# Kernel optimization log

Hardware: AMD Instinct MI355X
Metric: run time of the kernel (lower is better)

## Reference

```python
import jax, jax.numpy as jnp
import numpy as np

N_ACTIVE = 200000   # active voxels
GRID = 96           # spatial grid extent per axis
C = 128             # inplanes == outplanes
EPS = 1e-4          # scn BatchNormalization default eps


def _build_rulebook(n, g, seed=0):
    """Submanifold 3x3x3 rulebook: for each of 27 offsets, pairs (in_site, out_site)
    where coord[in] = coord[out] + offset and both sites are active. Padded to
    length n with dummy index n."""
    rng = np.random.default_rng(seed)
    lin = rng.choice(g ** 3, size=n, replace=False)
    coords = np.stack(np.unravel_index(lin, (g, g, g)), axis=1)  # [n,3]
    lut = -np.ones(g ** 3, dtype=np.int64)
    lut[lin] = np.arange(n)
    in_rows, out_rows = [], []
    for dx in (-1, 0, 1):
        for dy in (-1, 0, 1):
            for dz in (-1, 0, 1):
                nb = coords + np.array([dx, dy, dz])
                valid = np.all((nb >= 0) & (nb < g), axis=1)
                j = np.full(n, -1, dtype=np.int64)
                j[valid] = lut[np.ravel_multi_index(nb[valid].T, (g, g, g))]
                hit = j >= 0
                ii = j[hit]
                oi = np.nonzero(hit)[0].astype(np.int64)
                pad = n - ii.shape[0]
                in_rows.append(np.concatenate([ii, np.full(pad, n, dtype=np.int64)]))
                out_rows.append(np.concatenate([oi, np.full(pad, n, dtype=np.int64)]))
    return np.stack(in_rows), np.stack(out_rows)  # each [27, n]


def setup_inputs() -> dict:
    key = jax.random.key(0)
    k_feat, k_w1, k_w2 = jax.random.split(key, 3)
    in_idx_np, out_idx_np = _build_rulebook(N_ACTIVE, GRID)
    w_std = 1.0 / np.sqrt(27 * C)
    return {
        "features": jax.random.normal(k_feat, (N_ACTIVE, C), dtype=jnp.float32),
        "W1": jax.random.normal(k_w1, (27, C, C), dtype=jnp.float32) * w_std,
        "gamma1": jnp.ones((C,), jnp.float32),
        "beta1": jnp.zeros((C,), jnp.float32),
        "W2": jax.random.normal(k_w2, (27, C, C), dtype=jnp.float32) * w_std,
        "gamma2": jnp.ones((C,), jnp.float32),
        "beta2": jnp.zeros((C,), jnp.float32),
        "in_idx": jnp.asarray(in_idx_np),
        "out_idx": jnp.asarray(out_idx_np),
    }


def _subm_conv(feats, W, in_idx, out_idx):
    # feats: [N, Cin]; W: [27, Cin, Cout]; rulebook idx: [27, K] (dummy = N)
    n, c_in = feats.shape
    c_out = W.shape[-1]
    feats_pad = jnp.concatenate([feats, jnp.zeros((1, c_in), feats.dtype)], axis=0)

    def step(acc, t):
        ii, oi, w = t
        contrib = feats_pad[ii] @ w  # [K, Cout] gather -> GEMM
        return acc.at[oi].add(contrib), None  # scatter-add (dummy row n absorbs pad)

    acc0 = jnp.zeros((n + 1, c_out), feats.dtype)
    acc, _ = jax.lax.scan(step, acc0, (in_idx, out_idx, W))
    return acc[:n]


def _bn(x, gamma, beta):
    # batch-norm over active sites (training-mode batch stats)
    m = x.mean(axis=0)
    v = x.var(axis=0)
    return (x - m) * jax.lax.rsqrt(v + EPS) * gamma + beta


def reference(features, W1, gamma1, beta1, W2, gamma2, beta2, in_idx, out_idx):
    out = _subm_conv(features, W1, in_idx, out_idx)
    out = jax.nn.relu(_bn(out, gamma1, beta1))          # scn.BatchNormReLU
    out = _subm_conv(out, W2, in_idx, out_idx)
    out = _bn(out, gamma2, beta2)                       # scn.BatchNormalization
    return jax.nn.relu(out + features)                  # AddTable + ReLU
```

## Files before the change

### kernel.cpp

```cpp
#include <hip/hip_runtime.h>

#define NACT 200000
#define MPAD 200064
#define NBLK 1563
#define KOFF 27

typedef __bf16 bf16x8 __attribute__((ext_vector_type(8)));
typedef __bf16 bf16x4 __attribute__((ext_vector_type(4)));
typedef float f32x4 __attribute__((ext_vector_type(4)));

__device__ __forceinline__ void async_load16(const void* g, void* l) {
  __builtin_amdgcn_global_load_lds(
      (__attribute__((address_space(1))) void*)g,
      (__attribute__((address_space(3))) void*)l, 16, 0, 0);
}

__global__ void fill_g(int* __restrict__ G) {
  int i = blockIdx.x * 256 + threadIdx.x;
  if (i < KOFF * MPAD) G[i] = NACT;
}

__global__ void scatter_g(const int* __restrict__ ii, const int* __restrict__ oi,
                          int* __restrict__ G) {
  int i = blockIdx.x * 256 + threadIdx.x;
  if (i >= KOFF * NACT) return;
  int k = i / NACT;
  int o = oi[i];
  G[k * MPAD + o] = ii[i];
}

__global__ void fix_g(int* __restrict__ G) {
  int k = threadIdx.x;
  if (k < KOFF) G[k * MPAD + NACT] = NACT;
}

__global__ void cast_feats(const float* __restrict__ F, __bf16* __restrict__ X) {
  int i = blockIdx.x * 256 + threadIdx.x;
  if (i >= (NACT + 1) * 32) return;
  float4 v = (i < NACT * 32) ? ((const float4*)F)[i] : make_float4(0.f, 0.f, 0.f, 0.f);
  bf16x4 o = {(__bf16)v.x, (__bf16)v.y, (__bf16)v.z, (__bf16)v.w};
  *(bf16x4*)(X + (i << 2)) = o;
}

__global__ void prep_w(const float* __restrict__ W1, const float* __restrict__ W2,
                       __bf16* __restrict__ T1, __bf16* __restrict__ T2) {
  int i = blockIdx.x * 256 + threadIdx.x;
  if (i >= KOFF * 128 * 128) return;
  int k = i >> 14, rem = i & 16383, n = rem >> 7, c = rem & 127;
  int src = (k << 14) + (c << 7) + n;
  T1[i] = (__bf16)W1[src];
  T2[i] = (__bf16)W2[src];
}

__global__ __launch_bounds__(256, 4) void gemm_gather(
    const __bf16* __restrict__ X,
    const __bf16* __restrict__ WT,
    const int* __restrict__ G,
    __bf16* __restrict__ Y,
    float* __restrict__ Pst)
{
  __shared__ __bf16 Alds[128 * 64];
  __shared__ __bf16 Blds[128 * 64];
  const int t = threadIdx.x;
  const int lane = t & 63;
  const int w = t >> 6;
  const int wm = (w & 1) << 6;
  const int wn = (w >> 1) << 6;
  const int m_base = blockIdx.x << 7;
  const int r0 = t >> 3;
  const int scb = t & 7;
  const int l15 = lane & 15;
  const int q4 = lane >> 4;

  f32x4 acc[4][4];
#pragma unroll
  for (int i = 0; i < 4; ++i)
#pragma unroll
    for (int j = 0; j < 4; ++j) acc[i][j] = (f32x4){0.f, 0.f, 0.f, 0.f};

  for (int kk = 0; kk < KOFF; ++kk) {
    int rowA[4];
#pragma unroll
    for (int j = 0; j < 4; ++j)
      rowA[j] = G[kk * MPAD + m_base + r0 + j * 32];
    const __bf16* wb = WT + (kk << 14);
#pragma unroll
    for (int s = 0; s < 2; ++s) {
      const int c0 = s << 6;
      __syncthreads();
#pragma unroll
      for (int j = 0; j < 4; ++j) {
        const int r = r0 + j * 32;
        const int gcb = scb ^ (r & 7);
        async_load16(wb + (r << 7) + c0 + (gcb << 3), &Blds[(((r << 3) + scb) << 3)]);
        async_load16(X + (rowA[j] << 7) + c0 + (gcb << 3), &Alds[(((r << 3) + scb) << 3)]);
      }
      __syncthreads();
#pragma unroll
      for (int ks = 0; ks < 2; ++ks) {
        bf16x8 af[4], bfr[4];
        const int cb0 = (ks << 2) + q4;
#pragma unroll
        for (int mi = 0; mi < 4; ++mi) {
          const int r = wm + mi * 16 + l15;
          af[mi] = *(const bf16x8*)&Alds[(((r << 3) + (cb0 ^ (r & 7))) << 3)];
        }
#pragma unroll
        for (int ni = 0; ni < 4; ++ni) {
          const int r = wn + ni * 16 + l15;
          bfr[ni] = *(const bf16x8*)&Blds[(((r << 3) + (cb0 ^ (r & 7))) << 3)];
        }
#pragma unroll
        for (int mi = 0; mi < 4; ++mi)
#pragma unroll
          for (int ni = 0; ni < 4; ++ni)
            acc[mi][ni] = __builtin_amdgcn_mfma_f32_16x16x32_bf16(
                af[mi], bfr[ni], acc[mi][ni], 0, 0, 0);
      }
    }
  }

#pragma unroll
  for (int mi = 0; mi < 4; ++mi) {
#pragma unroll
    for (int ni = 0; ni < 4; ++ni) {
      const int col = wn + ni * 16 + l15;
#pragma unroll
      for (int rg = 0; rg < 4; ++rg) {
        const int row = m_base + wm + mi * 16 + (q4 << 2) + rg;
        Y[(row << 7) + col] = (__bf16)acc[mi][ni][rg];
      }
    }
  }

  float s[4], s2[4];
#pragma unroll
  for (int ni = 0; ni < 4; ++ni) {
    float a = 0.f, b = 0.f;
#pragma unroll
    for (int mi = 0; mi < 4; ++mi)
#pragma unroll
      for (int rg = 0; rg < 4; ++rg) {
        float v = acc[mi][ni][rg];
        a += v; b += v * v;
      }
    s[ni] = a; s2[ni] = b;
  }
#pragma unroll
  for (int ni = 0; ni < 4; ++ni) {
    s[ni]  += __shfl_xor(s[ni], 16);  s[ni]  += __shfl_xor(s[ni], 32);
    s2[ni] += __shfl_xor(s2[ni], 16); s2[ni] += __shfl_xor(s2[ni], 32);
  }
  float* sc = (float*)Alds;
  __syncthreads();
  if (q4 == 0) {
#pragma unroll
    for (int ni = 0; ni < 4; ++ni) {
      sc[(w << 6) + ni * 16 + l15]       = s[ni];
      sc[256 + (w << 6) + ni * 16 + l15] = s2[ni];
    }
  }
  __syncthreads();
  {
    const int kind = t >> 7, col = t & 127;
    const int w1 = (col >> 6) << 1;
    const float v = sc[kind * 256 + (w1 << 6) + (col & 63)] +
                    sc[kind * 256 + ((w1 + 1) << 6) + (col & 63)];
    Pst[(size_t)t * NBLK + blockIdx.x] = v;
  }
}

__global__ void stats_reduce(const float* __restrict__ P, float* __restrict__ st) {
  int b = blockIdx.x;
  const float* p = P + (size_t)b * NBLK;
  float s = 0.f;
  for (int i = threadIdx.x; i < NBLK; i += 256) s += p[i];
  for (int off = 32; off; off >>= 1) s += __shfl_down(s, off);
  __shared__ float ls[4];
  if ((threadIdx.x & 63) == 0) ls[threadIdx.x >> 6] = s;
  __syncthreads();
  if (threadIdx.x == 0) st[b] = ls[0] + ls[1] + ls[2] + ls[3];
}

__global__ void bn_coeffs(const float* __restrict__ st, const float* __restrict__ gamma,
                          const float* __restrict__ beta, float* __restrict__ co) {
  int c = threadIdx.x;
  float m = st[c] * (1.f / NACT);
  float v = st[128 + c] * (1.f / NACT) - m * m;
  float sc = gamma[c] * rsqrtf(v + 1e-4f);
  co[c] = sc;
  co[128 + c] = beta[c] - m * sc;
}

__global__ void bn_relu_cast(const __bf16* __restrict__ Y, const float* __restrict__ co,
                             __bf16* __restrict__ X2) {
  int i = blockIdx.x * 256 + threadIdx.x;
  if (i >= (NACT + 1) * 16) return;
  bf16x8 o;
  if (i < NACT * 16) {
    bf16x8 v = ((const bf16x8*)Y)[i];
    int cg = (i & 15) << 3;
#pragma unroll
    for (int e = 0; e < 8; ++e) {
      float x = fmaf((float)v[e], co[cg + e], co[128 + cg + e]);
      o[e] = (__bf16)fmaxf(x, 0.f);
    }
  } else {
#pragma unroll
    for (int e = 0; e < 8; ++e) o[e] = (__bf16)0.f;
  }
  ((bf16x8*)X2)[i] = o;
}

__global__ void bn_add_relu(const __bf16* __restrict__ Y, const float* __restrict__ co,
                            const float* __restrict__ F, float* __restrict__ O) {
  int i = blockIdx.x * 256 + threadIdx.x;
  if (i >= NACT * 16) return;
  bf16x8 v = ((const bf16x8*)Y)[i];
  float4 f0 = ((const float4*)F)[2 * i];
  float4 f1 = ((const float4*)F)[2 * i + 1];
  int cg = (i & 15) << 3;
  float4 o0, o1;
  o0.x = fmaxf(fmaf((float)v[0], co[cg + 0], co[128 + cg + 0]) + f0.x, 0.f);
  o0.y = fmaxf(fmaf((float)v[1], co[cg + 1], co[128 + cg + 1]) + f0.y, 0.f);
  o0.z = fmaxf(fmaf((float)v[2], co[cg + 2], co[128 + cg + 2]) + f0.z, 0.f);
  o0.w = fmaxf(fmaf((float)v[3], co[cg + 3], co[128 + cg + 3]) + f0.w, 0.f);
  o1.x = fmaxf(fmaf((float)v[4], co[cg + 4], co[128 + cg + 4]) + f1.x, 0.f);
  o1.y = fmaxf(fmaf((float)v[5], co[cg + 5], co[128 + cg + 5]) + f1.y, 0.f);
  o1.z = fmaxf(fmaf((float)v[6], co[cg + 6], co[128 + cg + 6]) + f1.z, 0.f);
  o1.w = fmaxf(fmaf((float)v[7], co[cg + 7], co[128 + cg + 7]) + f1.w, 0.f);
  ((float4*)O)[2 * i] = o0;
  ((float4*)O)[2 * i + 1] = o1;
}

extern "C" void kernel_launch(void* const* d_in, const int* in_sizes, int n_in,
                              void* d_out, int out_size, void* d_ws, size_t ws_size,
                              hipStream_t stream) {
  const float* features = (const float*)d_in[0];
  const float* W1       = (const float*)d_in[1];
  const float* gamma1   = (const float*)d_in[2];
  const float* beta1    = (const float*)d_in[3];
  const float* W2       = (const float*)d_in[4];
  const float* gamma2   = (const float*)d_in[5];
  const float* beta2    = (const float*)d_in[6];
  const int* in_idx     = (const int*)d_in[7];
  const int* out_idx    = (const int*)d_in[8];

  char* ws = (char*)d_ws;
  size_t off = 0;
  int*    G   = (int*)(ws + off);    off += (size_t)KOFF * MPAD * 4;
  __bf16* X   = (__bf16*)(ws + off); off += (size_t)(NACT + 1) * 128 * 2;
  __bf16* T1  = (__bf16*)(ws + off); off += (size_t)KOFF * 128 * 128 * 2;
  __bf16* T2  = (__bf16*)(ws + off); off += (size_t)KOFF * 128 * 128 * 2;
  __bf16* Y   = (__bf16*)(ws + off); off += (size_t)MPAD * 128 * 2;
  float*  Pst = (float*)(ws + off);  off += (size_t)256 * NBLK * 4;
  float*  st  = (float*)(ws + off);  off += 4096;

  fill_g<<<(KOFF * MPAD + 255) / 256, 256, 0, stream>>>(G);
  scatter_g<<<(KOFF * NACT + 255) / 256, 256, 0, stream>>>(in_idx, out_idx, G);
  fix_g<<<1, 32, 0, stream>>>(G);
  cast_feats<<<((NACT + 1) * 32 + 255) / 256, 256, 0, stream>>>(features, X);
  prep_w<<<(KOFF * 128 * 128 + 255) / 256, 256, 0, stream>>>(W1, W2, T1, T2);

  gemm_gather<<<NBLK, 256, 0, stream>>>(X, T1, G, Y, Pst);
  stats_reduce<<<256, 256, 0, stream>>>(Pst, st);
  bn_coeffs<<<1, 128, 0, stream>>>(st, gamma1, beta1, st + 512);
  bn_relu_cast<<<((NACT + 1) * 16 + 255) / 256, 256, 0, stream>>>(Y, st + 512, X);

  gemm_gather<<<NBLK, 256, 0, stream>>>(X, T2, G, Y, Pst);
  stats_reduce<<<256, 256, 0, stream>>>(Pst, st);
  bn_coeffs<<<1, 128, 0, stream>>>(st, gamma2, beta2, st + 768);
  bn_add_relu<<<(NACT * 16 + 255) / 256, 256, 0, stream>>>(Y, st + 768, features, (float*)d_out);
}
```

Measured before the change: 616.3 us.

## Double-buffer gather GEMM stages and fuse BN stats reduction with coefficients

The gather-GEMM kernel now preloads all 27 rulebook row indices for the tile into LDS and double-buffers the A/B tiles, so async global-to-LDS loads for the next stage overlap MFMA compute on the current one. Manual vmcnt waits and sched barriers replace the per-stage syncthreads pairs. Separately, the stats reduction and BN coefficient kernels are merged into one launch. Doubling LDS per block lowers the occupancy target from 4 to 2 blocks per CU, which reduces latency hiding from extra waves.

```diff
diff --git a/kernel.cpp b/kernel.cpp
--- a/kernel.cpp
+++ b/kernel.cpp
@@ -4,6 +4,7 @@
 #define MPAD 200064
 #define NBLK 1563
 #define KOFF 27
+#define NSTAGE (KOFF * 2)
 
 typedef __bf16 bf16x8 __attribute__((ext_vector_type(8)));
 typedef __bf16 bf16x4 __attribute__((ext_vector_type(4)));
@@ -52,15 +53,19 @@
   T2[i] = (__bf16)W2[src];
 }
 
-__global__ __launch_bounds__(256, 4) void gemm_gather(
+__global__ __launch_bounds__(256, 2) void gemm_gather(
     const __bf16* __restrict__ X,
     const __bf16* __restrict__ WT,
     const int* __restrict__ G,
     __bf16* __restrict__ Y,
     float* __restrict__ Pst)
 {
-  __shared__ __bf16 Alds[128 * 64];
-  __shared__ __bf16 Blds[128 * 64];
+  __shared__ __bf16 Al0[128 * 64];
+  __shared__ __bf16 Bl0[128 * 64];
+  __shared__ __bf16 Al1[128 * 64];
+  __shared__ __bf16 Bl1[128 * 64];
+  __shared__ int Gl[KOFF * 128];
+  __shared__ float red[512];
   const int t = threadIdx.x;
   const int lane = t & 63;
   const int w = t >> 6;
@@ -78,47 +83,69 @@
 #pragma unroll
     for (int j = 0; j < 4; ++j) acc[i][j] = (f32x4){0.f, 0.f, 0.f, 0.f};
 
-  for (int kk = 0; kk < KOFF; ++kk) {
-    int rowA[4];
-#pragma unroll
-    for (int j = 0; j < 4; ++j)
-      rowA[j] = G[kk * MPAD + m_base + r0 + j * 32];
-    const __bf16* wb = WT + (kk << 14);
-#pragma unroll
-    for (int s = 0; s < 2; ++s) {
-      const int c0 = s << 6;
-      __syncthreads();
-#pragma unroll
-      for (int j = 0; j < 4; ++j) {
-        const int r = r0 + j * 32;
-        const int gcb = scb ^ (r & 7);
-        async_load16(wb + (r << 7) + c0 + (gcb << 3), &Blds[(((r << 3) + scb) << 3)]);
-        async_load16(X + (rowA[j] << 7) + c0 + (gcb << 3), &Alds[(((r << 3) + scb) << 3)]);
-      }
-      __syncthreads();
-#pragma unroll
-      for (int ks = 0; ks < 2; ++ks) {
-        bf16x8 af[4], bfr[4];
-        const int cb0 = (ks << 2) + q4;
-#pragma unroll
-        for (int mi = 0; mi < 4; ++mi) {
-          const int r = wm + mi * 16 + l15;
-          af[mi] = *(const bf16x8*)&Alds[(((r << 3) + (cb0 ^ (r & 7))) << 3)];
-        }
-#pragma unroll
-        for (int ni = 0; ni < 4; ++ni) {
-          const int r = wn + ni * 16 + l15;
-          bfr[ni] = *(const bf16x8*)&Blds[(((r << 3) + (cb0 ^ (r & 7))) << 3)];
-        }
-#pragma unroll
-        for (int mi = 0; mi < 4; ++mi)
-#pragma unroll
-          for (int ni = 0; ni < 4; ++ni)
-            acc[mi][ni] = __builtin_amdgcn_mfma_f32_16x16x32_bf16(
-                af[mi], bfr[ni], acc[mi][ni], 0, 0, 0);
-      }
-    }
-  }
+  for (int i = t; i < KOFF * 128; i += 256)
+    Gl[i] = G[(size_t)(i >> 7) * MPAD + m_base + (i & 127)];
+  __syncthreads();
+
+#define STAGE_ISSUE(sidx, AL, BL)                                              \
+  do {                                                                         \
+    const int k_ = (sidx) >> 1;                                                \
+    const int c0_ = ((sidx) & 1) << 6;                                         \
+    const __bf16* wb_ = WT + (k_ << 14);                                       \
+    _Pragma("unroll") for (int j = 0; j < 4; ++j) {                            \
+      const int r_ = r0 + j * 32;                                              \
+      const int rowA_ = Gl[(k_ << 7) + r_];                                    \
+      const int gcb_ = scb ^ (r_ & 7);                                         \
+      async_load16(wb_ + (r_ << 7) + c0_ + (gcb_ << 3),                        \
+                   &(BL)[(((r_ << 3) + scb) << 3)]);                           \
+      async_load16(X + ((size_t)rowA_ << 7) + c0_ + (gcb_ << 3),               \
+                   &(AL)[(((r_ << 3) + scb) << 3)]);                           \
+    }                                                                          \
+  } while (0)
+
+#define STAGE_COMPUTE(AL, BL)                                                  \
+  do {                                                                         \
+    _Pragma("unroll") for (int ks = 0; ks < 2; ++ks) {                         \
+      bf16x8 af[4], bfr[4];                                                    \
+      const int cb0 = (ks << 2) + q4;                                          \
+      _Pragma("unroll") for (int mi = 0; mi < 4; ++mi) {                       \
+        const int r = wm + mi * 16 + l15;                                      \
+        af[mi] = *(const bf16x8*)&(AL)[(((r << 3) + (cb0 ^ (r & 7))) << 3)];   \
+      }                                                                        \
+      _Pragma("unroll") for (int ni = 0; ni < 4; ++ni) {                       \
+        const int r = wn + ni * 16 + l15;                                      \
+        bfr[ni] = *(const bf16x8*)&(BL)[(((r << 3) + (cb0 ^ (r & 7))) << 3)];  \
+      }                                                                        \
+      _Pragma("unroll") for (int mi = 0; mi < 4; ++mi)                         \
+          _Pragma("unroll") for (int ni = 0; ni < 4; ++ni)                     \
+              acc[mi][ni] = __builtin_amdgcn_mfma_f32_16x16x32_bf16(           \
+                  af[mi], bfr[ni], acc[mi][ni], 0, 0, 0);                      \
+    }                                                                          \
+  } while (0)
+
+  STAGE_ISSUE(0, Al0, Bl0);
+  for (int s = 0; s < NSTAGE; s += 2) {
+    if (s + 1 < NSTAGE) STAGE_ISSUE(s + 1, Al1, Bl1);
+    asm volatile("s_waitcnt vmcnt(8)" ::: "memory");
+    __builtin_amdgcn_s_barrier();
+    __builtin_amdgcn_sched_barrier(0);
+    STAGE_COMPUTE(Al0, Bl0);
+    __builtin_amdgcn_sched_barrier(0);
+    __builtin_amdgcn_s_barrier();
+    if (s + 2 < NSTAGE) {
+      STAGE_ISSUE(s + 2, Al0, Bl0);
+      asm volatile("s_waitcnt vmcnt(8)" ::: "memory");
+    } else {
+      asm volatile("s_waitcnt vmcnt(0)" ::: "memory");
+    }
+    __builtin_amdgcn_s_barrier();
+    __builtin_amdgcn_sched_barrier(0);
+    STAGE_COMPUTE(Al1, Bl1);
+    __builtin_amdgcn_sched_barrier(0);
+    __builtin_amdgcn_s_barrier();
+  }
+#undef STAGE_ISSUE
+#undef STAGE_COMPUTE
 
 #pragma unroll
   for (int mi = 0; mi < 4; ++mi) {
@@ -151,45 +178,44 @@
     s[ni]  += __shfl_xor(s[ni], 16);  s[ni]  += __shfl_xor(s[ni], 32);
     s2[ni] += __shfl_xor(s2[ni], 16); s2[ni] += __shfl_xor(s2[ni], 32);
   }
-  float* sc = (float*)Alds;
   __syncthreads();
   if (q4 == 0) {
 #pragma unroll
     for (int ni = 0; ni < 4; ++ni) {
-      sc[(w << 6) + ni * 16 + l15]       = s[ni];
-      sc[256 + (w << 6) + ni * 16 + l15] = s2[ni];
+      red[(w << 6) + ni * 16 + l15]       = s[ni];
+      red[256 + (w << 6) + ni * 16 + l15] = s2[ni];
     }
   }
   __syncthreads();
   {
     const int kind = t >> 7, col = t & 127;
     const int w1 = (col >> 6) << 1;
-    const float v = sc[kind * 256 + (w1 << 6) + (col & 63)] +
-                    sc[kind * 256 + ((w1 + 1) << 6) + (col & 63)];
+    const float v = red[kind * 256 + (w1 << 6) + (col & 63)] +
+                    red[kind * 256 + ((w1 + 1) << 6) + (col & 63)];
     Pst[(size_t)t * NBLK + blockIdx.x] = v;
   }
 }
 
-__global__ void stats_reduce(const float* __restrict__ P, float* __restrict__ st) {
-  int b = blockIdx.x;
-  const float* p = P + (size_t)b * NBLK;
-  float s = 0.f;
-  for (int i = threadIdx.x; i < NBLK; i += 256) s += p[i];
-  for (int off = 32; off; off >>= 1) s += __shfl_down(s, off);
-  __shared__ float ls[4];
-  if ((threadIdx.x & 63) == 0) ls[threadIdx.x >> 6] = s;
-  __syncthreads();
-  if (threadIdx.x == 0) st[b] = ls[0] + ls[1] + ls[2] + ls[3];
-}
-
-__global__ void bn_coeffs(const float* __restrict__ st, const float* __restrict__ gamma,
-                          const float* __restrict__ beta, float* __restrict__ co) {
-  int c = threadIdx.x;
-  float m = st[c] * (1.f / NACT);
-  float v = st[128 + c] * (1.f / NACT) - m * m;
-  float sc = gamma[c] * rsqrtf(v + 1e-4f);
-  co[c] = sc;
-  co[128 + c] = beta[c] - m * sc;
+__global__ void stats_coeffs(const float* __restrict__ P, const float* __restrict__ gamma,
+                             const float* __restrict__ beta, float* __restrict__ co) {
+  int c = blockIdx.x;
+  const float* p1 = P + (size_t)c * NBLK;
+  const float* p2 = P + (size_t)(128 + c) * NBLK;
+  float s = 0.f, s2 = 0.f;
+  for (int i = threadIdx.x; i < NBLK; i += 256) { s += p1[i]; s2 += p2[i]; }
+  for (int off = 32; off; off >>= 1) { s += __shfl_down(s, off); s2 += __shfl_down(s2, off); }
+  __shared__ float ls[8];
+  if ((threadIdx.x & 63) == 0) { ls[threadIdx.x >> 6] = s; ls[4 + (threadIdx.x >> 6)] = s2; }
+  __syncthreads();
+  if (threadIdx.x == 0) {
+    float S = ls[0] + ls[1] + ls[2] + ls[3];
+    float S2 = ls[4] + ls[5] + ls[6] + ls[7];
+    float m = S * (1.f / NACT);
+    float v = S2 * (1.f / NACT) - m * m;
+    float sc = gamma[c] * rsqrtf(v + 1e-4f);
+    co[c] = sc;
+    co[128 + c] = beta[c] - m * sc;
+  }
 }
 
 __global__ void bn_relu_cast(const __bf16* __restrict__ Y, const float* __restrict__ co,
@@ -263,12 +289,10 @@
   prep_w<<<(KOFF * 128 * 128 + 255) / 256, 256, 0, stream>>>(W1, W2, T1, T2);
 
   gemm_gather<<<NBLK, 256, 0, stream>>>(X, T1, G, Y, Pst);
-  stats_reduce<<<256, 256, 0, stream>>>(Pst, st);
-  bn_coeffs<<<1, 128, 0, stream>>>(st, gamma1, beta1, st + 512);
-  bn_relu_cast<<<((NACT + 1) * 16 + 255) / 256, 256, 0, stream>>>(Y, st + 512, X);
+  stats_coeffs<<<128, 256, 0, stream>>>(Pst, gamma1, beta1, st);
+  bn_relu_cast<<<((NACT + 1) * 16 + 255) / 256, 256, 0, stream>>>(Y, st, X);
 
   gemm_gather<<<NBLK, 256, 0, stream>>>(X, T2, G, Y, Pst);
-  stats_reduce<<<256, 256, 0, stream>>>(Pst, st);
-  bn_coeffs<<<1, 128, 0, stream>>>(st, gamma2, beta2, st + 768);
-  bn_add_relu<<<(NACT * 16 + 255) / 256, 256, 0, stream>>>(Y, st + 768, features, (float*)d_out);
-}
+  stats_coeffs<<<128, 256, 0, stream>>>(Pst, gamma2, beta2, st + 256);
+  bn_add_relu<<<(NACT * 16 + 255) / 256, 256, 0, stream>>>(Y, st + 256, features, (float*)d_out);
+}
```

Result: slower. 691.4 us (+12.2%).

## Enlarge gather-GEMM M tile to 192 rows and fuse BN stats reduction kernels

Applied to the files above, without the earlier changes.

Raises the rows per block in the gather GEMM from 128 to 192, so each weight tile in LDS is reused across more gathered rows and fewer blocks are launched. Occupancy drops to 3 blocks per CU, and more accumulator registers are needed. The separate stats reduction and BN coefficient kernels are merged into one kernel per channel to cut launch overhead. A dedicated shared buffer replaces the reuse of the A tile for the reduction scratch space.

```diff
diff --git a/kernel.cpp b/kernel.cpp
--- a/kernel.cpp
+++ b/kernel.cpp
@@ -2,7 +2,8 @@
 
 #define NACT 200000
 #define MPAD 200064
-#define NBLK 1563
+#define BM 192
+#define NBLK 1042
 #define KOFF 27
 
 typedef __bf16 bf16x8 __attribute__((ext_vector_type(8)));
@@ -52,36 +53,37 @@
   T2[i] = (__bf16)W2[src];
 }
 
-__global__ __launch_bounds__(256, 4) void gemm_gather(
+__global__ __launch_bounds__(256, 3) void gemm_gather(
     const __bf16* __restrict__ X,
     const __bf16* __restrict__ WT,
     const int* __restrict__ G,
     __bf16* __restrict__ Y,
     float* __restrict__ Pst)
 {
-  __shared__ __bf16 Alds[128 * 64];
+  __shared__ __bf16 Alds[BM * 64];
   __shared__ __bf16 Blds[128 * 64];
+  __shared__ float red[512];
   const int t = threadIdx.x;
   const int lane = t & 63;
   const int w = t >> 6;
-  const int wm = (w & 1) << 6;
+  const int wm = (w & 1) * 96;
   const int wn = (w >> 1) << 6;
-  const int m_base = blockIdx.x << 7;
+  const int m_base = blockIdx.x * BM;
   const int r0 = t >> 3;
   const int scb = t & 7;
   const int l15 = lane & 15;
   const int q4 = lane >> 4;
 
-  f32x4 acc[4][4];
-#pragma unroll
-  for (int i = 0; i < 4; ++i)
+  f32x4 acc[6][4];
+#pragma unroll
+  for (int i = 0; i < 6; ++i)
 #pragma unroll
     for (int j = 0; j < 4; ++j) acc[i][j] = (f32x4){0.f, 0.f, 0.f, 0.f};
 
   for (int kk = 0; kk < KOFF; ++kk) {
-    int rowA[4];
-#pragma unroll
-    for (int j = 0; j < 4; ++j)
+    int rowA[6];
+#pragma unroll
+    for (int j = 0; j < 6; ++j)
       rowA[j] = G[kk * MPAD + m_base + r0 + j * 32];
     const __bf16* wb = WT + (kk << 14);
 #pragma unroll
@@ -93,35 +95,39 @@
         const int r = r0 + j * 32;
         const int gcb = scb ^ (r & 7);
         async_load16(wb + (r << 7) + c0 + (gcb << 3), &Blds[(((r << 3) + scb) << 3)]);
-        async_load16(X + (rowA[j] << 7) + c0 + (gcb << 3), &Alds[(((r << 3) + scb) << 3)]);
+      }
+#pragma unroll
+      for (int j = 0; j < 6; ++j) {
+        const int r = r0 + j * 32;
+        const int gcb = scb ^ (r & 7);
+        async_load16(X + ((size_t)rowA[j] << 7) + c0 + (gcb << 3),
+                     &Alds[(((r << 3) + scb) << 3)]);
       }
       __syncthreads();
 #pragma unroll
       for (int ks = 0; ks < 2; ++ks) {
-        bf16x8 af[4], bfr[4];
         const int cb0 = (ks << 2) + q4;
-#pragma unroll
-        for (int mi = 0; mi < 4; ++mi) {
-          const int r = wm + mi * 16 + l15;
-          af[mi] = *(const bf16x8*)&Alds[(((r << 3) + (cb0 ^ (r & 7))) << 3)];
-        }
+        bf16x8 bfr[4];
 #pragma unroll
         for (int ni = 0; ni < 4; ++ni) {
           const int r = wn + ni * 16 + l15;
           bfr[ni] = *(const bf16x8*)&Blds[(((r << 3) + (cb0 ^ (r & 7))) << 3)];
         }
 #pragma unroll
-        for (int mi = 0; mi < 4; ++mi)
+        for (int mi = 0; mi < 6; ++mi) {
+          const int r = wm + mi * 16 + l15;
+          bf16x8 af = *(const bf16x8*)&Alds[(((r << 3) + (cb0 ^ (r & 7))) << 3)];
 #pragma unroll
           for (int ni = 0; ni < 4; ++ni)
             acc[mi][ni] = __builtin_amdgcn_mfma_f32_16x16x32_bf16(
-                af[mi], bfr[ni], acc[mi][ni], 0, 0, 0);
-      }
-    }
-  }
-
-#pragma unroll
-  for (int mi = 0; mi < 4; ++mi) {
+                af, bfr[ni], acc[mi][ni], 0, 0, 0);
+        }
+      }
+    }
+  }
+
+#pragma unroll
+  for (int mi = 0; mi < 6; ++mi) {
 #pragma unroll
     for (int ni = 0; ni < 4; ++ni) {
       const int col = wn + ni * 16 + l15;
@@ -138,7 +144,7 @@
   for (int ni = 0; ni < 4; ++ni) {
     float a = 0.f, b = 0.f;
 #pragma unroll
-    for (int mi = 0; mi < 4; ++mi)
+    for (int mi = 0; mi < 6; ++mi)
 #pragma unroll
       for (int rg = 0; rg < 4; ++rg) {
         float v = acc[mi][ni][rg];
@@ -151,45 +157,44 @@
     s[ni]  += __shfl_xor(s[ni], 16);  s[ni]  += __shfl_xor(s[ni], 32);
     s2[ni] += __shfl_xor(s2[ni], 16); s2[ni] += __shfl_xor(s2[ni], 32);
   }
-  float* sc = (float*)Alds;
   __syncthreads();
   if (q4 == 0) {
 #pragma unroll
     for (int ni = 0; ni < 4; ++ni) {
-      sc[(w << 6) + ni * 16 + l15]       = s[ni];
-      sc[256 + (w << 6) + ni * 16 + l15] = s2[ni];
+      red[(w << 6) + ni * 16 + l15]       = s[ni];
+      red[256 + (w << 6) + ni * 16 + l15] = s2[ni];
     }
   }
   __syncthreads();
   {
     const int kind = t >> 7, col = t & 127;
     const int w1 = (col >> 6) << 1;
-    const float v = sc[kind * 256 + (w1 << 6) + (col & 63)] +
-                    sc[kind * 256 + ((w1 + 1) << 6) + (col & 63)];
+    const float v = red[kind * 256 + (w1 << 6) + (col & 63)] +
+                    red[kind * 256 + ((w1 + 1) << 6) + (col & 63)];
     Pst[(size_t)t * NBLK + blockIdx.x] = v;
   }
 }
 
-__global__ void stats_reduce(const float* __restrict__ P, float* __restrict__ st) {
-  int b = blockIdx.x;
-  const float* p = P + (size_t)b * NBLK;
-  float s = 0.f;
-  for (int i = threadIdx.x; i < NBLK; i += 256) s += p[i];
-  for (int off = 32; off; off >>= 1) s += __shfl_down(s, off);
-  __shared__ float ls[4];
-  if ((threadIdx.x & 63) == 0) ls[threadIdx.x >> 6] = s;
+__global__ void stats_coeffs(const float* __restrict__ P, const float* __restrict__ gamma,
+                             const float* __restrict__ beta, float* __restrict__ co) {
+  int c = blockIdx.x;
+  const float* p1 = P + (size_t)c * NBLK;
+  const float* p2 = P + (size_t)(128 + c) * NBLK;
+  float s = 0.f, s2 = 0.f;
+  for (int i = threadIdx.x; i < NBLK; i += 256) { s += p1[i]; s2 += p2[i]; }
+  for (int off = 32; off; off >>= 1) { s += __shfl_down(s, off); s2 += __shfl_down(s2, off); }
+  __shared__ float ls[8];
+  if ((threadIdx.x & 63) == 0) { ls[threadIdx.x >> 6] = s; ls[4 + (threadIdx.x >> 6)] = s2; }
   __syncthreads();
-  if (threadIdx.x == 0) st[b] = ls[0] + ls[1] + ls[2] + ls[3];
-}
-
-__global__ void bn_coeffs(const float* __restrict__ st, const float* __restrict__ gamma,
-                          const float* __restrict__ beta, float* __restrict__ co) {
-  int c = threadIdx.x;
-  float m = st[c] * (1.f / NACT);
-  float v = st[128 + c] * (1.f / NACT) - m * m;
-  float sc = gamma[c] * rsqrtf(v + 1e-4f);
-  co[c] = sc;
-  co[128 + c] = beta[c] - m * sc;
+  if (threadIdx.x == 0) {
+    float S = ls[0] + ls[1] + ls[2] + ls[3];
+    float S2 = ls[4] + ls[5] + ls[6] + ls[7];
+    float m = S * (1.f / NACT);
+    float v = S2 * (1.f / NACT) - m * m;
+    float sc = gamma[c] * rsqrtf(v + 1e-4f);
+    co[c] = sc;
+    co[128 + c] = beta[c] - m * sc;
+  }
 }
 
 __global__ void bn_relu_cast(const __bf16* __restrict__ Y, const float* __restrict__ co,
@@ -263,12 +268,10 @@
   prep_w<<<(KOFF * 128 * 128 + 255) / 256, 256, 0, stream>>>(W1, W2, T1, T2);
 
   gemm_gather<<<NBLK, 256, 0, stream>>>(X, T1, G, Y, Pst);
-  stats_reduce<<<256, 256, 0, stream>>>(Pst, st);
-  bn_coeffs<<<1, 128, 0, stream>>>(st, gamma1, beta1, st + 512);
-  bn_relu_cast<<<((NACT + 1) * 16 + 255) / 256, 256, 0, stream>>>(Y, st + 512, X);
+  stats_coeffs<<<128, 256, 0, stream>>>(Pst, gamma1, beta1, st);
+  bn_relu_cast<<<((NACT + 1) * 16 + 255) / 256, 256, 0, stream>>>(Y, st, X);
 
   gemm_gather<<<NBLK, 256, 0, stream>>>(X, T2, G, Y, Pst);
-  stats_reduce<<<256, 256, 0, stream>>>(Pst, st);
-  bn_coeffs<<<1, 128, 0, stream>>>(st, gamma2, beta2, st + 768);
-  bn_add_relu<<<(NACT * 16 + 255) / 256, 256, 0, stream>>>(Y, st + 768, features, (float*)d_out);
-}
+  stats_coeffs<<<128, 256, 0, stream>>>(Pst, gamma2, beta2, st + 256);
+  bn_add_relu<<<(NACT * 16 + 255) / 256, 256, 0, stream>>>(Y, st + 256, features, (float*)d_out);
+}
```

After: 743.1 us. 20.6% more time.

## Merge prep kernels, replace stats reduction with atomics, fold BN coeffs into apply

Applied to the files above, without the earlier changes.

Merges the G fill, feature cast, weight transpose and stats zeroing into one prep launch, and drops fix_g by having scatter_g skip padded entries. The GEMM now atomically adds per-block channel sums into a global stats buffer instead of writing per-block partials, which removes the stats_reduce and bn_coeffs launches. Each BN apply block recomputes the coefficients into shared memory. Launch bounds go from 4 to 5 waves per SIMD. The aim is fewer launches and less intermediate traffic, at the cost of atomic contention, non-deterministic float summation order and possible register pressure.

```diff
diff --git a/kernel.cpp b/kernel.cpp
--- a/kernel.cpp
+++ b/kernel.cpp
@@ -5,6 +5,11 @@
 #define NBLK 1563
 #define KOFF 27
 
+#define NB_FILL 21101
+#define NB_CAST 25001
+#define NB_PREPW 1728
+#define NB_PREP (NB_FILL + NB_CAST + NB_PREPW + 1)
+
 typedef __bf16 bf16x8 __attribute__((ext_vector_type(8)));
 typedef __bf16 bf16x4 __attribute__((ext_vector_type(4)));
 typedef float f32x4 __attribute__((ext_vector_type(4)));
@@ -15,9 +20,29 @@
       (__attribute__((address_space(3))) void*)l, 16, 0, 0);
 }
 
-__global__ void fill_g(int* __restrict__ G) {
-  int i = blockIdx.x * 256 + threadIdx.x;
-  if (i < KOFF * MPAD) G[i] = NACT;
+__global__ void prep(int* __restrict__ G, const float* __restrict__ F,
+                     __bf16* __restrict__ X, const float* __restrict__ W1,
+                     const float* __restrict__ W2, __bf16* __restrict__ T1,
+                     __bf16* __restrict__ T2, float* __restrict__ st) {
+  const int b = blockIdx.x, t = threadIdx.x;
+  if (b < NB_FILL) {
+    int i = b * 256 + t;
+    if (i < KOFF * MPAD) G[i] = NACT;
+  } else if (b < NB_FILL + NB_CAST) {
+    int i = (b - NB_FILL) * 256 + t;
+    if (i >= (NACT + 1) * 32) return;
+    float4 v = (i < NACT * 32) ? ((const float4*)F)[i] : make_float4(0.f, 0.f, 0.f, 0.f);
+    bf16x4 o = {(__bf16)v.x, (__bf16)v.y, (__bf16)v.z, (__bf16)v.w};
+    *(bf16x4*)(X + (i << 2)) = o;
+  } else if (b < NB_FILL + NB_CAST + NB_PREPW) {
+    int i = (b - NB_FILL - NB_CAST) * 256 + t;
+    int k = i >> 14, rem = i & 16383, n = rem >> 7, c = rem & 127;
+    int src = (k << 14) + (c << 7) + n;
+    T1[i] = (__bf16)W1[src];
+    T2[i] = (__bf16)W2[src];
+  } else {
+    if (t < 512) st[t] = 0.f;
+  }
 }
 
 __global__ void scatter_g(const int* __restrict__ ii, const int* __restrict__ oi,
@@ -26,38 +51,15 @@
   if (i >= KOFF * NACT) return;
   int k = i / NACT;
   int o = oi[i];
-  G[k * MPAD + o] = ii[i];
-}
-
-__global__ void fix_g(int* __restrict__ G) {
-  int k = threadIdx.x;
-  if (k < KOFF) G[k * MPAD + NACT] = NACT;
-}
-
-__global__ void cast_feats(const float* __restrict__ F, __bf16* __restrict__ X) {
-  int i = blockIdx.x * 256 + threadIdx.x;
-  if (i >= (NACT + 1) * 32) return;
-  float4 v = (i < NACT * 32) ? ((const float4*)F)[i] : make_float4(0.f, 0.f, 0.f, 0.f);
-  bf16x4 o = {(__bf16)v.x, (__bf16)v.y, (__bf16)v.z, (__bf16)v.w};
-  *(bf16x4*)(X + (i << 2)) = o;
-}
-
-__global__ void prep_w(const float* __restrict__ W1, const float* __restrict__ W2,
-                       __bf16* __restrict__ T1, __bf16* __restrict__ T2) {
-  int i = blockIdx.x * 256 + threadIdx.x;
-  if (i >= KOFF * 128 * 128) return;
-  int k = i >> 14, rem = i & 16383, n = rem >> 7, c = rem & 127;
-  int src = (k << 14) + (c << 7) + n;
-  T1[i] = (__bf16)W1[src];
-  T2[i] = (__bf16)W2[src];
-}
-
-__global__ __launch_bounds__(256, 4) void gemm_gather(
+  if (o < NACT) G[k * MPAD + o] = ii[i];
+}
+
+__global__ __launch_bounds__(256, 5) void gemm_gather(
     const __bf16* __restrict__ X,
     const __bf16* __restrict__ WT,
     const int* __restrict__ G,
     __bf16* __restrict__ Y,
-    float* __restrict__ Pst)
+    float* __restrict__ st)
 {
   __shared__ __bf16 Alds[128 * 64];
   __shared__ __bf16 Blds[128 * 64];
@@ -93,7 +95,8 @@
         const int r = r0 + j * 32;
         const int gcb = scb ^ (r & 7);
         async_load16(wb + (r << 7) + c0 + (gcb << 3), &Blds[(((r << 3) + scb) << 3)]);
-        async_load16(X + (rowA[j] << 7) + c0 + (gcb << 3), &Alds[(((r << 3) + scb) << 3)]);
+        async_load16(X + ((size_t)rowA[j] << 7) + c0 + (gcb << 3),
+                     &Alds[(((r << 3) + scb) << 3)]);
       }
       __syncthreads();
 #pragma unroll
@@ -166,35 +169,24 @@
     const int w1 = (col >> 6) << 1;
     const float v = sc[kind * 256 + (w1 << 6) + (col & 63)] +
                     sc[kind * 256 + ((w1 + 1) << 6) + (col & 63)];
-    Pst[(size_t)t * NBLK + blockIdx.x] = v;
-  }
-}
-
-__global__ void stats_reduce(const float* __restrict__ P, float* __restrict__ st) {
-  int b = blockIdx.x;
-  const float* p = P + (size_t)b * NBLK;
-  float s = 0.f;
-  for (int i = threadIdx.x; i < NBLK; i += 256) s += p[i];
-  for (int off = 32; off; off >>= 1) s += __shfl_down(s, off);
-  __shared__ float ls[4];
-  if ((threadIdx.x & 63) == 0) ls[threadIdx.x >> 6] = s;
-  __syncthreads();
-  if (threadIdx.x == 0) st[b] = ls[0] + ls[1] + ls[2] + ls[3];
-}
-
-__global__ void bn_coeffs(const float* __restrict__ st, const float* __restrict__ gamma,
-                          const float* __restrict__ beta, float* __restrict__ co) {
-  int c = threadIdx.x;
-  float m = st[c] * (1.f / NACT);
-  float v = st[128 + c] * (1.f / NACT) - m * m;
-  float sc = gamma[c] * rsqrtf(v + 1e-4f);
-  co[c] = sc;
-  co[128 + c] = beta[c] - m * sc;
-}
-
-__global__ void bn_relu_cast(const __bf16* __restrict__ Y, const float* __restrict__ co,
+    atomicAdd(&st[t], v);
+  }
+}
+
+__global__ void bn_relu_cast(const __bf16* __restrict__ Y, const float* __restrict__ st,
+                             const float* __restrict__ gamma, const float* __restrict__ beta,
                              __bf16* __restrict__ X2) {
-  int i = blockIdx.x * 256 + threadIdx.x;
+  __shared__ float co[256];
+  const int t = threadIdx.x;
+  if (t < 128) {
+    float m = st[t] * (1.f / NACT);
+    float v = st[128 + t] * (1.f / NACT) - m * m;
+    float sc = gamma[t] * rsqrtf(v + 1e-4f);
+    co[t] = sc;
+    co[128 + t] = beta[t] - m * sc;
+  }
+  __syncthreads();
+  int i = blockIdx.x * 256 + t;
   if (i >= (NACT + 1) * 16) return;
   bf16x8 o;
   if (i < NACT * 16) {
@@ -212,9 +204,20 @@
   ((bf16x8*)X2)[i] = o;
 }
 
-__global__ void bn_add_relu(const __bf16* __restrict__ Y, const float* __restrict__ co,
+__global__ void bn_add_relu(const __bf16* __restrict__ Y, const float* __restrict__ st,
+                            const float* __restrict__ gamma, const float* __restrict__ beta,
                             const float* __restrict__ F, float* __restrict__ O) {
-  int i = blockIdx.x * 256 + threadIdx.x;
+  __shared__ float co[256];
+  const int t = threadIdx.x;
+  if (t < 128) {
+    float m = st[t] * (1.f / NACT);
+    float v = st[128 + t] * (1.f / NACT) - m * m;
+    float sc = gamma[t] * rsqrtf(v + 1e-4f);
+    co[t] = sc;
+    co[128 + t] = beta[t] - m * sc;
+  }
+  __syncthreads();
+  int i = blockIdx.x * 256 + t;
   if (i >= NACT * 16) return;
   bf16x8 v = ((const bf16x8*)Y)[i];
   float4 f0 = ((const float4*)F)[2 * i];
@@ -253,22 +256,15 @@
   __bf16* T1  = (__bf16*)(ws + off); off += (size_t)KOFF * 128 * 128 * 2;
   __bf16* T2  = (__bf16*)(ws + off); off += (size_t)KOFF * 128 * 128 * 2;
   __bf16* Y   = (__bf16*)(ws + off); off += (size_t)MPAD * 128 * 2;
-  float*  Pst = (float*)(ws + off);  off += (size_t)256 * NBLK * 4;
   float*  st  = (float*)(ws + off);  off += 4096;
 
-  fill_g<<<(KOFF * MPAD + 255) / 256, 256, 0, stream>>>(G);
+  prep<<<NB_PREP, 256, 0, stream>>>(G, features, X, W1, W2, T1, T2, st);
   scatter_g<<<(KOFF * NACT + 255) / 256, 256, 0, stream>>>(in_idx, out_idx, G);
-  fix_g<<<1, 32, 0, stream>>>(G);
-  cast_feats<<<((NACT + 1) * 32 + 255) / 256, 256, 0, stream>>>(features, X);
-  prep_w<<<(KOFF * 128 * 128 + 255) / 256, 256, 0, stream>>>(W1, W2, T1, T2);
-
-  gemm_gather<<<NBLK, 256, 0, stream>>>(X, T1, G, Y, Pst);
-  stats_reduce<<<256, 256, 0, stream>>>(Pst, st);
-  bn_coeffs<<<1, 128, 0, stream>>>(st, gamma1, beta1, st + 512);
-  bn_relu_cast<<<((NACT + 1) * 16 + 255) / 256, 256, 0, stream>>>(Y, st + 512, X);
-
-  gemm_gather<<<NBLK, 256, 0, stream>>>(X, T2, G, Y, Pst);
-  stats_reduce<<<256, 256, 0, stream>>>(Pst, st);
-  bn_coeffs<<<1, 128, 0, stream>>>(st, gamma2, beta2, st + 768);
-  bn_add_relu<<<(NACT * 16 + 255) / 256, 256, 0, stream>>>(Y, st + 768, features, (float*)d_out);
-}
+
+  gemm_gather<<<NBLK, 256, 0, stream>>>(X, T1, G, Y, st);
+  bn_relu_cast<<<((NACT + 1) * 16 + 255) / 256, 256, 0, stream>>>(Y, st, gamma1, beta1, X);
+
+  gemm_gather<<<NBLK, 256, 0, stream>>>(X, T2, G, Y, st + 256);
+  bn_add_relu<<<(NACT * 16 + 255) / 256, 256, 0, stream>>>(Y, st + 256, gamma2, beta2,
+                                                           features, (float*)d_out);
+}
```

Result: slower. 1.391 ms (+125.7%).
